# Performance work log

Measured on AMD Instinct MI355X. Metric: run time of the kernel, lower is better.

## Reference

```python
import jax, jax.numpy as jnp
import numpy as np

DIM = 1024
INTER = 512
E = 16            # n_routed_experts
TOPK = 4          # n_activated_experts
N_GROUPS = 4
TOPK_GROUPS = 2
ROUTE_SCALE = 1.0
INIT_STD = 0.02
B, S = 2, 1024


def setup_inputs() -> dict:
    key = jax.random.key(0)
    ks = jax.random.split(key, 8)
    return {
        "x": jax.random.normal(ks[0], (B, S, DIM), jnp.float32),
        "gate_w": jax.random.normal(ks[1], (E, DIM), jnp.float32) * INIT_STD,
        "gate_bias": jnp.zeros((E,), jnp.float32),
        "w1": jax.random.normal(ks[2], (E, INTER, DIM), jnp.float32) * INIT_STD,
        "w2": jax.random.normal(ks[3], (E, DIM, INTER), jnp.float32) * INIT_STD,
        "w3": jax.random.normal(ks[4], (E, INTER, DIM), jnp.float32) * INIT_STD,
        "ws1": jax.random.normal(ks[5], (INTER, DIM), jnp.float32) * INIT_STD,
        "ws2": jax.random.normal(ks[6], (DIM, INTER), jnp.float32) * INIT_STD,
        "ws3": jax.random.normal(ks[7], (INTER, DIM), jnp.float32) * INIT_STD,
    }


def reference(x, gate_w, gate_bias, w1, w2, w3, ws1, ws2, ws3):
    Bx, Sx, D = x.shape
    T = Bx * Sx
    xf = x.reshape(T, D)

    # ---- Gate: sigmoid scores + expert bias, group-limited top-k ----
    scores = jax.nn.sigmoid(xf @ gate_w.T)          # [T, E]
    original_scores = scores
    s = scores + gate_bias                          # bias only affects selection
    sg = s.reshape(T, N_GROUPS, E // N_GROUPS)
    group_scores = sg.max(axis=-1)                  # [T, G]
    _, gidx = jax.lax.top_k(group_scores, TOPK_GROUPS)
    keep = jnp.zeros((T, N_GROUPS), bool).at[jnp.arange(T)[:, None], gidx].set(True)
    s_masked = jnp.where(keep[:, :, None], sg, -jnp.inf).reshape(T, E)
    _, idx = jax.lax.top_k(s_masked, TOPK)          # [T, topk]
    weights = jnp.take_along_axis(original_scores, idx, axis=1) * ROUTE_SCALE

    # combine weights as sparse [T, E] matrix (scatter of top-k weights)
    comb = jnp.zeros((T, E), x.dtype).at[jnp.arange(T)[:, None], idx].add(weights)

    # ---- Routed experts: SwiGLU per expert, weighted combine ----
    h1 = jnp.einsum('td,eid->tei', xf, w1)          # [T, E, inter]
    h3 = jnp.einsum('td,eid->tei', xf, w3)
    h = jax.nn.silu(h1) * h3
    y = jnp.einsum('tei,edi,te->td', h, w2, comb)   # weighted combine

    # ---- Shared expert (SwiGLU MLP) ----
    z = (jax.nn.silu(xf @ ws1.T) * (xf @ ws3.T)) @ ws2.T

    return (y + z).reshape(Bx, Sx, D)
```

## Files before the change

### kernel.cpp

```cpp
#include <hip/hip_runtime.h>

#define T_TOK  2048
#define DIMD   1024
#define INTERI 512
#define NEXP   16
#define NSEG   17

typedef __bf16 bf16x8 __attribute__((ext_vector_type(8)));
typedef float  f32x4  __attribute__((ext_vector_type(4)));

__device__ __forceinline__ unsigned short f2b(float f) {
    union { float f; unsigned int u; } c; c.f = f;
    unsigned int u = c.u;
    unsigned int r = (u + 0x7FFFu + ((u >> 16) & 1u)) >> 16;
    return (unsigned short)r;
}

__device__ __forceinline__ void lds_barrier() {
    asm volatile("s_waitcnt lgkmcnt(0)" ::: "memory");
    __builtin_amdgcn_s_barrier();
}

__global__ __launch_bounds__(256) void cvt_all_kernel(
    const float* __restrict__ x,  const float* __restrict__ w1,
    const float* __restrict__ w3, const float* __restrict__ w2,
    const float* __restrict__ ws1, const float* __restrict__ ws3,
    const float* __restrict__ ws2,
    unsigned short* __restrict__ xb,  unsigned short* __restrict__ w1b,
    unsigned short* __restrict__ w3b, unsigned short* __restrict__ w2b,
    unsigned short* __restrict__ ws1b, unsigned short* __restrict__ ws3b,
    unsigned short* __restrict__ ws2b)
{
    int g = blockIdx.x * 256 + threadIdx.x;
    const float* s; unsigned short* d; int i;
    if      (g < 524288)  { s = x;   d = xb;   i = g; }
    else if (g < 2621440) { s = w1;  d = w1b;  i = g - 524288; }
    else if (g < 4718592) { s = w3;  d = w3b;  i = g - 2621440; }
    else if (g < 6815744) { s = w2;  d = w2b;  i = g - 4718592; }
    else if (g < 6946816) { s = ws1; d = ws1b; i = g - 6815744; }
    else if (g < 7077888) { s = ws3; d = ws3b; i = g - 6946816; }
    else                  { s = ws2; d = ws2b; i = g - 7077888; }
    float4 v = ((const float4*)s)[i];
    ushort4 o;
    o.x = f2b(v.x); o.y = f2b(v.y); o.z = f2b(v.z); o.w = f2b(v.w);
    ((ushort4*)d)[i] = o;
}

__global__ __launch_bounds__(256) void gate_score_kernel(
    const float* __restrict__ x, const float* __restrict__ gw,
    const float* __restrict__ gb,
    unsigned* __restrict__ sel, float4* __restrict__ selw)
{
    int tok  = blockIdx.x * 4 + (threadIdx.x >> 6);
    int lane = threadIdx.x & 63;
    const float* xp = x + (size_t)tok * DIMD;
    float xv[16];
#pragma unroll
    for (int j = 0; j < 16; ++j) xv[j] = xp[j * 64 + lane];

    float sc[16];
#pragma unroll
    for (int e = 0; e < 16; ++e) {
        const float* gwe = gw + e * DIMD;
        float p0 = 0.f, p1 = 0.f;
#pragma unroll
        for (int j = 0; j < 16; j += 2) {
            p0 += xv[j]     * gwe[j * 64 + lane];
            p1 += xv[j + 1] * gwe[(j + 1) * 64 + lane];
        }
        float p = p0 + p1;
#pragma unroll
        for (int o = 32; o; o >>= 1) p += __shfl_xor(p, o, 64);
        sc[e] = p;
    }
    if (lane != 0) return;

    float orig[16], s[16];
#pragma unroll
    for (int e = 0; e < 16; ++e) {
        orig[e] = 1.f / (1.f + expf(-sc[e]));
        s[e] = orig[e] + gb[e];
    }
    float gmax[4];
#pragma unroll
    for (int g = 0; g < 4; ++g) {
        float m = s[4 * g];
        for (int j = 1; j < 4; ++j) m = fmaxf(m, s[4 * g + j]);
        gmax[g] = m;
    }
    int g0 = 0;
    for (int g = 1; g < 4; ++g) if (gmax[g] > gmax[g0]) g0 = g;
    int g1 = -1;
    for (int g = 0; g < 4; ++g) { if (g == g0) continue; if (g1 < 0 || gmax[g] > gmax[g1]) g1 = g; }
    unsigned keep = (0xFu << (4 * g0)) | (0xFu << (4 * g1));
    unsigned used = 0;
    unsigned pk = 0;
    float w4[4];
    for (int j = 0; j < 4; ++j) {
        int best = -1;
        for (int e = 0; e < 16; ++e) {
            if (!((keep >> e) & 1u) || ((used >> e) & 1u)) continue;
            if (best < 0 || s[e] > s[best]) best = e;
        }
        used |= 1u << best;
        pk |= ((unsigned)best) << (4 * j);
        w4[j] = orig[best];
    }
    sel[tok] = pk;
    selw[tok] = make_float4(w4[0], w4[1], w4[2], w4[3]);
}

__global__ __launch_bounds__(256) void build_lists_kernel(
    const unsigned* __restrict__ sel, const float4* __restrict__ selw,
    int* __restrict__ counts, int* __restrict__ lst, float* __restrict__ lstw)
{
    const int e    = blockIdx.x;
    const int tid  = threadIdx.x;
    const int wave = tid >> 6;
    const int lane = tid & 63;

    __shared__ int wsum[4];
    __shared__ int basev;
    if (tid == 0) basev = 0;
    __syncthreads();

    for (int c = 0; c < T_TOK / 256; ++c) {
        int t = c * 256 + tid;
        unsigned s = sel[t];
        int match = -1;
#pragma unroll
        for (int j = 0; j < 4; ++j)
            if (((s >> (4 * j)) & 15u) == (unsigned)e) match = j;
        unsigned long long m = __ballot(match >= 0);
        int wpre = __popcll(m & ((1ull << lane) - 1ull));
        if (lane == 0) wsum[wave] = __popcll(m);
        __syncthreads();
        int pre = basev;
        for (int wv = 0; wv < wave; ++wv) pre += wsum[wv];
        if (match >= 0) {
            int pos = pre + wpre;
            lst [e * T_TOK + pos] = t | (match << 16);
            const float* wp = (const float*)&selw[t];
            lstw[e * T_TOK + pos] = wp[match];
        }
        __syncthreads();
        if (tid == 0) basev += wsum[0] + wsum[1] + wsum[2] + wsum[3];
        __syncthreads();
    }
    if (tid == 0) counts[e] = basev;
}

__global__ __launch_bounds__(256, 4) void gemm1_kernel(
    const unsigned short* __restrict__ xb,
    const unsigned short* __restrict__ w1b,
    const unsigned short* __restrict__ w3b,
    const unsigned short* __restrict__ ws1b,
    const unsigned short* __restrict__ ws3b,
    const int* __restrict__ counts,
    const int* __restrict__ lst,
    unsigned short* __restrict__ H)
{
    int b = blockIdx.x;
    int seg, mt, nt;
    if (b < 2048) {
        int xcd = b & 7, slot = b >> 3;
        seg = xcd + 8 * (slot >> 7);
        int tile = slot & 127;
        nt = tile & 3; mt = tile >> 2;
    } else {
        seg = NEXP;
        int tile = b - 2048;
        nt = tile & 3; mt = tile >> 2;
    }
    const int n_e = (seg == NEXP) ? T_TOK : counts[seg];
    const int m0  = mt * 64;
    if (m0 >= n_e) return;
    const int n0  = nt * 128;

    const unsigned short* w1p = (seg == NEXP) ? ws1b : w1b + (size_t)seg * INTERI * DIMD;
    const unsigned short* w3p = (seg == NEXP) ? ws3b : w3b + (size_t)seg * INTERI * DIMD;
    const int* lste = lst + seg * T_TOK;

    __shared__ __align__(16) unsigned short lA [2][64][32];
    __shared__ __align__(16) unsigned short lB1[2][128][32];
    __shared__ __align__(16) unsigned short lB3[2][128][32];

    const int tid  = threadIdx.x;
    const int wave = tid >> 6;
    const int lane = tid & 63;
    const int r4   = tid >> 2;
    const int skg  = (tid & 3) * 8;

    int ra = m0 + r4; if (ra > n_e - 1) ra = n_e - 1;
    int tok = (seg == NEXP) ? ra : (lste[ra] & 0xFFFF);
    const unsigned short* gA   = xb  + (size_t)tok * DIMD + skg;
    const unsigned short* gB1a = w1p + (size_t)(n0 + r4) * DIMD + skg;
    const unsigned short* gB1b = w1p + (size_t)(n0 + r4 + 64) * DIMD + skg;
    const unsigned short* gB3a = w3p + (size_t)(n0 + r4) * DIMD + skg;
    const unsigned short* gB3b = w3p + (size_t)(n0 + r4 + 64) * DIMD + skg;

    bf16x8 pa[2], pb1a[2], pb1b[2], pb3a[2], pb3b[2];

#define G1LOAD(k0) do { _Pragma("unroll") for (int kk = 0; kk < 2; ++kk) { \
    pa  [kk] = *(const bf16x8*)(gA   + (k0) + kk * 32); \
    pb1a[kk] = *(const bf16x8*)(gB1a + (k0) + kk * 32); \
    pb1b[kk] = *(const bf16x8*)(gB1b + (k0) + kk * 32); \
    pb3a[kk] = *(const bf16x8*)(gB3a + (k0) + kk * 32); \
    pb3b[kk] = *(const bf16x8*)(gB3b + (k0) + kk * 32); } } while (0)

#define G1STORE() do { _Pragma("unroll") for (int kk = 0; kk < 2; ++kk) { \
    *(bf16x8*)&lA [kk][r4][skg]      = pa  [kk]; \
    *(bf16x8*)&lB1[kk][r4][skg]      = pb1a[kk]; \
    *(bf16x8*)&lB1[kk][64 + r4][skg] = pb1b[kk]; \
    *(bf16x8*)&lB3[kk][r4][skg]      = pb3a[kk]; \
    *(bf16x8*)&lB3[kk][64 + r4][skg] = pb3b[kk]; } } while (0)

    f32x4 acc1[2][4], acc3[2][4];
    const f32x4 zero = {0.f, 0.f, 0.f, 0.f};
#pragma unroll
    for (int i = 0; i < 2; ++i)
#pragma unroll
        for (int j = 0; j < 4; ++j) { acc1[i][j] = zero; acc3[i][j] = zero; }

    const int wm   = (wave & 1) * 32;
    const int wn   = (wave >> 1) * 64;
    const int quad = lane >> 4;
    const int lrow = lane & 15;

    G1LOAD(0);
    const int NK = DIMD / 64;
    for (int it = 0; it < NK; ++it) {
        G1STORE();
        lds_barrier();
        if (it + 1 < NK) G1LOAD((it + 1) * 64);
#pragma unroll
        for (int kk = 0; kk < 2; ++kk) {
            bf16x8 a[2], b1[4], b3[4];
#pragma unroll
            for (int t = 0; t < 2; ++t)
                a[t] = *(const bf16x8*)&lA[kk][wm + t * 16 + lrow][quad * 8];
#pragma unroll
            for (int t = 0; t < 4; ++t) {
                b1[t] = *(const bf16x8*)&lB1[kk][wn + t * 16 + lrow][quad * 8];
                b3[t] = *(const bf16x8*)&lB3[kk][wn + t * 16 + lrow][quad * 8];
            }
#pragma unroll
            for (int i = 0; i < 2; ++i)
#pragma unroll
                for (int j = 0; j < 4; ++j) {
                    acc1[i][j] = __builtin_amdgcn_mfma_f32_16x16x32_bf16(a[i], b1[j], acc1[i][j], 0, 0, 0);
                    acc3[i][j] = __builtin_amdgcn_mfma_f32_16x16x32_bf16(a[i], b3[j], acc3[i][j], 0, 0, 0);
                }
        }
        lds_barrier();
    }
#undef G1LOAD
#undef G1STORE

    unsigned short* Hseg = H + (size_t)seg * T_TOK * INTERI;
#pragma unroll
    for (int i = 0; i < 2; ++i) {
        int rbase = m0 + wm + i * 16 + quad * 4;
#pragma unroll
        for (int r = 0; r < 4; ++r) {
            int row = rbase + r;
            if (row >= n_e) continue;
            unsigned short* hrow = Hseg + (size_t)row * INTERI + n0 + wn + lrow;
#pragma unroll
            for (int j = 0; j < 4; ++j) {
                float v1 = acc1[i][j][r];
                float v3 = acc3[i][j][r];
                float hv = (v1 / (1.f + __expf(-v1))) * v3;
                hrow[j * 16] = f2b(hv);
            }
        }
    }
}

__global__ __launch_bounds__(256, 4) void gemm2_kernel(
    const unsigned short* __restrict__ H,
    const unsigned short* __restrict__ w2b,
    const unsigned short* __restrict__ ws2b,
    const int* __restrict__ counts,
    const int* __restrict__ lst,
    const float* __restrict__ lstw,
    float* __restrict__ P)
{
    int b = blockIdx.x;
    int seg, mt, nt;
    if (b < 4096) {
        int xcd = b & 7, slot = b >> 3;
        seg = xcd + 8 * (slot >> 8);
        int tile = slot & 255;
        nt = tile & 7; mt = tile >> 3;
    } else {
        seg = NEXP;
        int tile = b - 4096;
        nt = tile & 7; mt = tile >> 3;
    }
    const int n_e = (seg == NEXP) ? T_TOK : counts[seg];
    const int m0  = mt * 64;
    if (m0 >= n_e) return;
    const int n0  = nt * 128;

    const unsigned short* w2p  = (seg == NEXP) ? ws2b : w2b + (size_t)seg * DIMD * INTERI;
    const unsigned short* Hseg = H + (size_t)seg * T_TOK * INTERI;

    __shared__ __align__(16) unsigned short lA[2][64][32];
    __shared__ __align__(16) unsigned short lB[2][128][32];

    const int tid  = threadIdx.x;
    const int wave = tid >> 6;
    const int lane = tid & 63;
    const int r4   = tid >> 2;
    const int skg  = (tid & 3) * 8;

    int ra = m0 + r4; if (ra > n_e - 1) ra = n_e - 1;
    const unsigned short* gA  = Hseg + (size_t)ra * INTERI + skg;
    const unsigned short* gB0 = w2p + (size_t)(n0 + r4) * INTERI + skg;
    const unsigned short* gB1 = w2p + (size_t)(n0 + r4 + 64) * INTERI + skg;

    bf16x8 pa[2], pb0[2], pb1[2];

#define G2LOAD(k0) do { _Pragma("unroll") for (int kk = 0; kk < 2; ++kk) { \
    pa [kk] = *(const bf16x8*)(gA  + (k0) + kk * 32); \
    pb0[kk] = *(const bf16x8*)(gB0 + (k0) + kk * 32); \
    pb1[kk] = *(const bf16x8*)(gB1 + (k0) + kk * 32); } } while (0)

#define G2STORE() do { _Pragma("unroll") for (int kk = 0; kk < 2; ++kk) { \
    *(bf16x8*)&lA[kk][r4][skg]      = pa [kk]; \
    *(bf16x8*)&lB[kk][r4][skg]      = pb0[kk]; \
    *(bf16x8*)&lB[kk][64 + r4][skg] = pb1[kk]; } } while (0)

    f32x4 acc[2][4];
    const f32x4 zero = {0.f, 0.f, 0.f, 0.f};
#pragma unroll
    for (int i = 0; i < 2; ++i)
#pragma unroll
        for (int j = 0; j < 4; ++j) acc[i][j] = zero;

    const int wm   = (wave & 1) * 32;
    const int wn   = (wave >> 1) * 64;
    const int quad = lane >> 4;
    const int lrow = lane & 15;

    G2LOAD(0);
    const int NK = INTERI / 64;
    for (int it = 0; it < NK; ++it) {
        G2STORE();
        lds_barrier();
        if (it + 1 < NK) G2LOAD((it + 1) * 64);
#pragma unroll
        for (int kk = 0; kk < 2; ++kk) {
            bf16x8 a[2], bv[4];
#pragma unroll
            for (int t = 0; t < 2; ++t)
                a[t] = *(const bf16x8*)&lA[kk][wm + t * 16 + lrow][quad * 8];
#pragma unroll
            for (int t = 0; t < 4; ++t)
                bv[t] = *(const bf16x8*)&lB[kk][wn + t * 16 + lrow][quad * 8];
#pragma unroll
            for (int i = 0; i < 2; ++i)
#pragma unroll
                for (int j = 0; j < 4; ++j)
                    acc[i][j] = __builtin_amdgcn_mfma_f32_16x16x32_bf16(a[i], bv[j], acc[i][j], 0, 0, 0);
        }
        lds_barrier();
    }
#undef G2LOAD
#undef G2STORE

#pragma unroll
    for (int i = 0; i < 2; ++i) {
        int rbase = m0 + wm + i * 16 + quad * 4;
#pragma unroll
        for (int r = 0; r < 4; ++r) {
            int row = rbase + r;
            if (row >= n_e) continue;
            int tok, slot; float wt;
            if (seg == NEXP) { tok = row; slot = 4; wt = 1.f; }
            else {
                int ent = lst[seg * T_TOK + row];
                tok = ent & 0xFFFF; slot = ent >> 16;
                wt = lstw[seg * T_TOK + row];
            }
            float* prow = P + ((size_t)slot * T_TOK + tok) * DIMD + n0 + wn + lrow;
#pragma unroll
            for (int j = 0; j < 4; ++j)
                prow[j * 16] = wt * acc[i][j][r];
        }
    }
}

__global__ __launch_bounds__(256) void combine_kernel(
    const float4* __restrict__ P, float4* __restrict__ y)
{
    const int i = blockIdx.x * 256 + threadIdx.x;
    const size_t plane = (size_t)T_TOK * DIMD / 4;
    float4 a = P[i];
    float4 b = P[plane + i];
    float4 c = P[2 * plane + i];
    float4 d = P[3 * plane + i];
    float4 e = P[4 * plane + i];
    float4 o;
    o.x = a.x + b.x + c.x + d.x + e.x;
    o.y = a.y + b.y + c.y + d.y + e.y;
    o.z = a.z + b.z + c.z + d.z + e.z;
    o.w = a.w + b.w + c.w + d.w + e.w;
    y[i] = o;
}

extern "C" void kernel_launch(void* const* d_in, const int* in_sizes, int n_in,
                              void* d_out, int out_size, void* d_ws, size_t ws_size,
                              hipStream_t stream)
{
    const float* x   = (const float*)d_in[0];
    const float* gw  = (const float*)d_in[1];
    const float* gb  = (const float*)d_in[2];
    const float* w1  = (const float*)d_in[3];
    const float* w2  = (const float*)d_in[4];
    const float* w3  = (const float*)d_in[5];
    const float* ws1 = (const float*)d_in[6];
    const float* ws2 = (const float*)d_in[7];
    const float* ws3 = (const float*)d_in[8];

    char* base = (char*)d_ws;
    size_t off = 0;
    auto alloc = [&](size_t bytes) {
        char* q = base + off; off += (bytes + 255) & ~(size_t)255; return q;
    };
    unsigned short* xb   = (unsigned short*)alloc((size_t)T_TOK * DIMD * 2);
    unsigned short* w1b  = (unsigned short*)alloc((size_t)NEXP * INTERI * DIMD * 2);
    unsigned short* w3b  = (unsigned short*)alloc((size_t)NEXP * INTERI * DIMD * 2);
    unsigned short* w2b  = (unsigned short*)alloc((size_t)NEXP * DIMD * INTERI * 2);
    unsigned short* ws1b = (unsigned short*)alloc((size_t)INTERI * DIMD * 2);
    unsigned short* ws3b = (unsigned short*)alloc((size_t)INTERI * DIMD * 2);
    unsigned short* ws2b = (unsigned short*)alloc((size_t)DIMD * INTERI * 2);
    unsigned short* Hb   = (unsigned short*)alloc((size_t)NSEG * T_TOK * INTERI * 2);
    int*            cnts = (int*)alloc(NEXP * 4);
    int*            lstp = (int*)alloc((size_t)NEXP * T_TOK * 4);
    float*          lstw = (float*)alloc((size_t)NEXP * T_TOK * 4);
    unsigned*       selp = (unsigned*)alloc((size_t)T_TOK * 4);
    float4*         selw = (float4*)alloc((size_t)T_TOK * 16);
    float*          Pb   = (float*)alloc((size_t)5 * T_TOK * DIMD * 4);

    cvt_all_kernel<<<28160, 256, 0, stream>>>(x, w1, w3, w2, ws1, ws3, ws2,
                                              xb, w1b, w3b, w2b, ws1b, ws3b, ws2b);
    gate_score_kernel<<<T_TOK / 4, 256, 0, stream>>>(x, gw, gb, selp, selw);
    build_lists_kernel<<<NEXP, 256, 0, stream>>>(selp, selw, cnts, lstp, lstw);
    gemm1_kernel<<<2176, 256, 0, stream>>>(xb, w1b, w3b, ws1b, ws3b, cnts, lstp, Hb);
    gemm2_kernel<<<4352, 256, 0, stream>>>(Hb, w2b, ws2b, cnts, lstp, lstw, Pb);
    combine_kernel<<<(T_TOK * DIMD / 4) / 256, 256, 0, stream>>>((const float4*)Pb, (float4*)d_out);
}
```

Baseline: 257.8 us.

## Enlarge GEMM M-tile to 128 rows and swizzle LDS columns

Both grouped GEMMs move from 64x128 to 128x128 block tiles, so each wave computes a 64x64 sub-tile with twice the accumulators. The aim is more reuse of each weight tile loaded into LDS and fewer redundant weight reads from global memory. An XOR-style swizzle on the 8-element LDS column groups is added to cut bank conflicts on the fragment reads. The cost is higher register pressure (launch bounds occupancy lowered from 4 to 2), half as many blocks, and more wasted work on partially filled tiles for experts with few tokens.

```diff
diff --git a/kernel.cpp b/kernel.cpp
--- a/kernel.cpp
+++ b/kernel.cpp
@@ -8,6 +8,8 @@
 
 typedef __bf16 bf16x8 __attribute__((ext_vector_type(8)));
 typedef float  f32x4  __attribute__((ext_vector_type(4)));
+
+#define SW(row, c) ((((c) + ((row) >> 1)) & 3) * 8)
 
 __device__ __forceinline__ unsigned short f2b(float f) {
     union { float f; unsigned int u; } c; c.f = f;
@@ -150,7 +152,7 @@
     if (tid == 0) counts[e] = basev;
 }
 
-__global__ __launch_bounds__(256, 4) void gemm1_kernel(
+__global__ __launch_bounds__(256, 2) void gemm1_kernel(
     const unsigned short* __restrict__ xb,
     const unsigned short* __restrict__ w1b,
     const unsigned short* __restrict__ w3b,
@@ -162,18 +164,18 @@
 {
     int b = blockIdx.x;
     int seg, mt, nt;
-    if (b < 2048) {
+    if (b < 1024) {
         int xcd = b & 7, slot = b >> 3;
-        seg = xcd + 8 * (slot >> 7);
-        int tile = slot & 127;
-        nt = tile & 3; mt = tile >> 2;
+        seg = xcd + 8 * (slot >> 6);
+        int tile = slot & 63;
+        mt = tile >> 2; nt = tile & 3;
     } else {
         seg = NEXP;
-        int tile = b - 2048;
-        nt = tile & 3; mt = tile >> 2;
+        int tile = b - 1024;
+        mt = tile >> 2; nt = tile & 3;
     }
     const int n_e = (seg == NEXP) ? T_TOK : counts[seg];
-    const int m0  = mt * 64;
+    const int m0  = mt * 128;
     if (m0 >= n_e) return;
     const int n0  = nt * 128;
 
@@ -181,51 +183,56 @@
     const unsigned short* w3p = (seg == NEXP) ? ws3b : w3b + (size_t)seg * INTERI * DIMD;
     const int* lste = lst + seg * T_TOK;
 
-    __shared__ __align__(16) unsigned short lA [2][64][32];
+    __shared__ __align__(16) unsigned short lA [2][128][32];
     __shared__ __align__(16) unsigned short lB1[2][128][32];
     __shared__ __align__(16) unsigned short lB3[2][128][32];
 
     const int tid  = threadIdx.x;
     const int wave = tid >> 6;
     const int lane = tid & 63;
-    const int r4   = tid >> 2;
-    const int skg  = (tid & 3) * 8;
-
-    int ra = m0 + r4; if (ra > n_e - 1) ra = n_e - 1;
-    int tok = (seg == NEXP) ? ra : (lste[ra] & 0xFFFF);
-    const unsigned short* gA   = xb  + (size_t)tok * DIMD + skg;
-    const unsigned short* gB1a = w1p + (size_t)(n0 + r4) * DIMD + skg;
-    const unsigned short* gB1b = w1p + (size_t)(n0 + r4 + 64) * DIMD + skg;
-    const unsigned short* gB3a = w3p + (size_t)(n0 + r4) * DIMD + skg;
-    const unsigned short* gB3b = w3p + (size_t)(n0 + r4 + 64) * DIMD + skg;
-
-    bf16x8 pa[2], pb1a[2], pb1b[2], pb3a[2], pb3b[2];
-
-#define G1LOAD(k0) do { _Pragma("unroll") for (int kk = 0; kk < 2; ++kk) { \
-    pa  [kk] = *(const bf16x8*)(gA   + (k0) + kk * 32); \
-    pb1a[kk] = *(const bf16x8*)(gB1a + (k0) + kk * 32); \
-    pb1b[kk] = *(const bf16x8*)(gB1b + (k0) + kk * 32); \
-    pb3a[kk] = *(const bf16x8*)(gB3a + (k0) + kk * 32); \
-    pb3b[kk] = *(const bf16x8*)(gB3b + (k0) + kk * 32); } } while (0)
-
-#define G1STORE() do { _Pragma("unroll") for (int kk = 0; kk < 2; ++kk) { \
-    *(bf16x8*)&lA [kk][r4][skg]      = pa  [kk]; \
-    *(bf16x8*)&lB1[kk][r4][skg]      = pb1a[kk]; \
-    *(bf16x8*)&lB1[kk][64 + r4][skg] = pb1b[kk]; \
-    *(bf16x8*)&lB3[kk][r4][skg]      = pb3a[kk]; \
-    *(bf16x8*)&lB3[kk][64 + r4][skg] = pb3b[kk]; } } while (0)
-
-    f32x4 acc1[2][4], acc3[2][4];
-    const f32x4 zero = {0.f, 0.f, 0.f, 0.f};
-#pragma unroll
-    for (int i = 0; i < 2; ++i)
-#pragma unroll
-        for (int j = 0; j < 4; ++j) { acc1[i][j] = zero; acc3[i][j] = zero; }
-
-    const int wm   = (wave & 1) * 32;
-    const int wn   = (wave >> 1) * 64;
     const int quad = lane >> 4;
     const int lrow = lane & 15;
+    const int r4   = tid >> 2;
+    const int ct   = tid & 3;
+
+    int ra0 = m0 + r4;       if (ra0 > n_e - 1) ra0 = n_e - 1;
+    int ra1 = m0 + r4 + 64;  if (ra1 > n_e - 1) ra1 = n_e - 1;
+    int tok0 = (seg == NEXP) ? ra0 : (lste[ra0] & 0xFFFF);
+    int tok1 = (seg == NEXP) ? ra1 : (lste[ra1] & 0xFFFF);
+    const unsigned short* gA0  = xb  + (size_t)tok0 * DIMD + ct * 8;
+    const unsigned short* gA1  = xb  + (size_t)tok1 * DIMD + ct * 8;
+    const unsigned short* gB1a = w1p + (size_t)(n0 + r4)      * DIMD + ct * 8;
+    const unsigned short* gB1b = w1p + (size_t)(n0 + r4 + 64) * DIMD + ct * 8;
+    const unsigned short* gB3a = w3p + (size_t)(n0 + r4)      * DIMD + ct * 8;
+    const unsigned short* gB3b = w3p + (size_t)(n0 + r4 + 64) * DIMD + ct * 8;
+
+    bf16x8 pa[2][2], pb1[2][2], pb3[2][2];
+
+#define G1LOAD(k0) do { _Pragma("unroll") for (int kk = 0; kk < 2; ++kk) { \
+    pa [0][kk] = *(const bf16x8*)(gA0  + (k0) + kk * 32); \
+    pa [1][kk] = *(const bf16x8*)(gA1  + (k0) + kk * 32); \
+    pb1[0][kk] = *(const bf16x8*)(gB1a + (k0) + kk * 32); \
+    pb1[1][kk] = *(const bf16x8*)(gB1b + (k0) + kk * 32); \
+    pb3[0][kk] = *(const bf16x8*)(gB3a + (k0) + kk * 32); \
+    pb3[1][kk] = *(const bf16x8*)(gB3b + (k0) + kk * 32); } } while (0)
+
+#define G1STORE() do { _Pragma("unroll") for (int kk = 0; kk < 2; ++kk) { \
+    *(bf16x8*)&lA [kk][r4]     [SW(r4, ct)]      = pa [0][kk]; \
+    *(bf16x8*)&lA [kk][64 + r4][SW(64 + r4, ct)] = pa [1][kk]; \
+    *(bf16x8*)&lB1[kk][r4]     [SW(r4, ct)]      = pb1[0][kk]; \
+    *(bf16x8*)&lB1[kk][64 + r4][SW(64 + r4, ct)] = pb1[1][kk]; \
+    *(bf16x8*)&lB3[kk][r4]     [SW(r4, ct)]      = pb3[0][kk]; \
+    *(bf16x8*)&lB3[kk][64 + r4][SW(64 + r4, ct)] = pb3[1][kk]; } } while (0)
+
+    f32x4 acc1[4][4], acc3[4][4];
+    const f32x4 zero = {0.f, 0.f, 0.f, 0.f};
+#pragma unroll
+    for (int i = 0; i < 4; ++i)
+#pragma unroll
+        for (int j = 0; j < 4; ++j) { acc1[i][j] = zero; acc3[i][j] = zero; }
+
+    const int wm = (wave & 1) * 64;
+    const int wn = (wave >> 1) * 64;
 
     G1LOAD(0);
     const int NK = DIMD / 64;
@@ -235,17 +242,20 @@
         if (it + 1 < NK) G1LOAD((it + 1) * 64);
 #pragma unroll
         for (int kk = 0; kk < 2; ++kk) {
-            bf16x8 a[2], b1[4], b3[4];
-#pragma unroll
-            for (int t = 0; t < 2; ++t)
-                a[t] = *(const bf16x8*)&lA[kk][wm + t * 16 + lrow][quad * 8];
+            bf16x8 a[4], b1[4], b3[4];
 #pragma unroll
             for (int t = 0; t < 4; ++t) {
-                b1[t] = *(const bf16x8*)&lB1[kk][wn + t * 16 + lrow][quad * 8];
-                b3[t] = *(const bf16x8*)&lB3[kk][wn + t * 16 + lrow][quad * 8];
-            }
-#pragma unroll
-            for (int i = 0; i < 2; ++i)
+                int rr = wm + t * 16 + lrow;
+                a[t] = *(const bf16x8*)&lA[kk][rr][SW(rr, quad)];
+            }
+#pragma unroll
+            for (int t = 0; t < 4; ++t) {
+                int rc = wn + t * 16 + lrow;
+                b1[t] = *(const bf16x8*)&lB1[kk][rc][SW(rc, quad)];
+                b3[t] = *(const bf16x8*)&lB3[kk][rc][SW(rc, quad)];
+            }
+#pragma unroll
+            for (int i = 0; i < 4; ++i)
 #pragma unroll
                 for (int j = 0; j < 4; ++j) {
                     acc1[i][j] = __builtin_amdgcn_mfma_f32_16x16x32_bf16(a[i], b1[j], acc1[i][j], 0, 0, 0);
@@ -259,7 +269,7 @@
 
     unsigned short* Hseg = H + (size_t)seg * T_TOK * INTERI;
 #pragma unroll
-    for (int i = 0; i < 2; ++i) {
+    for (int i = 0; i < 4; ++i) {
         int rbase = m0 + wm + i * 16 + quad * 4;
 #pragma unroll
         for (int r = 0; r < 4; ++r) {
@@ -277,7 +287,7 @@
     }
 }
 
-__global__ __launch_bounds__(256, 4) void gemm2_kernel(
+__global__ __launch_bounds__(256, 2) void gemm2_kernel(
     const unsigned short* __restrict__ H,
     const unsigned short* __restrict__ w2b,
     const unsigned short* __restrict__ ws2b,
@@ -288,61 +298,65 @@
 {
     int b = blockIdx.x;
     int seg, mt, nt;
-    if (b < 4096) {
+    if (b < 2048) {
         int xcd = b & 7, slot = b >> 3;
-        seg = xcd + 8 * (slot >> 8);
-        int tile = slot & 255;
-        nt = tile & 7; mt = tile >> 3;
+        seg = xcd + 8 * (slot >> 7);
+        int tile = slot & 127;
+        mt = tile >> 3; nt = tile & 7;
     } else {
         seg = NEXP;
-        int tile = b - 4096;
-        nt = tile & 7; mt = tile >> 3;
+        int tile = b - 2048;
+        mt = tile >> 3; nt = tile & 7;
     }
     const int n_e = (seg == NEXP) ? T_TOK : counts[seg];
-    const int m0  = mt * 64;
+    const int m0  = mt * 128;
     if (m0 >= n_e) return;
     const int n0  = nt * 128;
 
     const unsigned short* w2p  = (seg == NEXP) ? ws2b : w2b + (size_t)seg * DIMD * INTERI;
     const unsigned short* Hseg = H + (size_t)seg * T_TOK * INTERI;
 
-    __shared__ __align__(16) unsigned short lA[2][64][32];
+    __shared__ __align__(16) unsigned short lA[2][128][32];
     __shared__ __align__(16) unsigned short lB[2][128][32];
 
     const int tid  = threadIdx.x;
     const int wave = tid >> 6;
     const int lane = tid & 63;
-    const int r4   = tid >> 2;
-    const int skg  = (tid & 3) * 8;
-
-    int ra = m0 + r4; if (ra > n_e - 1) ra = n_e - 1;
-    const unsigned short* gA  = Hseg + (size_t)ra * INTERI + skg;
-    const unsigned short* gB0 = w2p + (size_t)(n0 + r4) * INTERI + skg;
-    const unsigned short* gB1 = w2p + (size_t)(n0 + r4 + 64) * INTERI + skg;
-
-    bf16x8 pa[2], pb0[2], pb1[2];
-
-#define G2LOAD(k0) do { _Pragma("unroll") for (int kk = 0; kk < 2; ++kk) { \
-    pa [kk] = *(const bf16x8*)(gA  + (k0) + kk * 32); \
-    pb0[kk] = *(const bf16x8*)(gB0 + (k0) + kk * 32); \
-    pb1[kk] = *(const bf16x8*)(gB1 + (k0) + kk * 32); } } while (0)
-
-#define G2STORE() do { _Pragma("unroll") for (int kk = 0; kk < 2; ++kk) { \
-    *(bf16x8*)&lA[kk][r4][skg]      = pa [kk]; \
-    *(bf16x8*)&lB[kk][r4][skg]      = pb0[kk]; \
-    *(bf16x8*)&lB[kk][64 + r4][skg] = pb1[kk]; } } while (0)
-
-    f32x4 acc[2][4];
-    const f32x4 zero = {0.f, 0.f, 0.f, 0.f};
-#pragma unroll
-    for (int i = 0; i < 2; ++i)
-#pragma unroll
-        for (int j = 0; j < 4; ++j) acc[i][j] = zero;
-
-    const int wm   = (wave & 1) * 32;
-    const int wn   = (wave >> 1) * 64;
     const int quad = lane >> 4;
     const int lrow = lane & 15;
+    const int r4   = tid >> 2;
+    const int ct   = tid & 3;
+
+    int ra0 = m0 + r4;       if (ra0 > n_e - 1) ra0 = n_e - 1;
+    int ra1 = m0 + r4 + 64;  if (ra1 > n_e - 1) ra1 = n_e - 1;
+    const unsigned short* gA0 = Hseg + (size_t)ra0 * INTERI + ct * 8;
+    const unsigned short* gA1 = Hseg + (size_t)ra1 * INTERI + ct * 8;
+    const unsigned short* gB0 = w2p + (size_t)(n0 + r4)      * INTERI + ct * 8;
+    const unsigned short* gB1 = w2p + (size_t)(n0 + r4 + 64) * INTERI + ct * 8;
+
+    bf16x8 pa[2][2], pb[2][2];
+
+#define G2LOAD(k0) do { _Pragma("unroll") for (int kk = 0; kk < 2; ++kk) { \
+    pa[0][kk] = *(const bf16x8*)(gA0 + (k0) + kk * 32); \
+    pa[1][kk] = *(const bf16x8*)(gA1 + (k0) + kk * 32); \
+    pb[0][kk] = *(const bf16x8*)(gB0 + (k0) + kk * 32); \
+    pb[1][kk] = *(const bf16x8*)(gB1 + (k0) + kk * 32); } } while (0)
+
+#define G2STORE() do { _Pragma("unroll") for (int kk = 0; kk < 2; ++kk) { \
+    *(bf16x8*)&lA[kk][r4]     [SW(r4, ct)]      = pa[0][kk]; \
+    *(bf16x8*)&lA[kk][64 + r4][SW(64 + r4, ct)] = pa[1][kk]; \
+    *(bf16x8*)&lB[kk][r4]     [SW(r4, ct)]      = pb[0][kk]; \
+    *(bf16x8*)&lB[kk][64 + r4][SW(64 + r4, ct)] = pb[1][kk]; } } while (0)
+
+    f32x4 acc[4][4];
+    const f32x4 zero = {0.f, 0.f, 0.f, 0.f};
+#pragma unroll
+    for (int i = 0; i < 4; ++i)
+#pragma unroll
+        for (int j = 0; j < 4; ++j) acc[i][j] = zero;
+
+    const int wm = (wave & 1) * 64;
+    const int wn = (wave >> 1) * 64;
 
     G2LOAD(0);
     const int NK = INTERI / 64;
@@ -352,15 +366,19 @@
         if (it + 1 < NK) G2LOAD((it + 1) * 64);
 #pragma unroll
         for (int kk = 0; kk < 2; ++kk) {
-            bf16x8 a[2], bv[4];
-#pragma unroll
-            for (int t = 0; t < 2; ++t)
-                a[t] = *(const bf16x8*)&lA[kk][wm + t * 16 + lrow][quad * 8];
-#pragma unroll
-            for (int t = 0; t < 4; ++t)
-                bv[t] = *(const bf16x8*)&lB[kk][wn + t * 16 + lrow][quad * 8];
-#pragma unroll
-            for (int i = 0; i < 2; ++i)
+            bf16x8 a[4], bv[4];
+#pragma unroll
+            for (int t = 0; t < 4; ++t) {
+                int rr = wm + t * 16 + lrow;
+                a[t] = *(const bf16x8*)&lA[kk][rr][SW(rr, quad)];
+            }
+#pragma unroll
+            for (int t = 0; t < 4; ++t) {
+                int rc = wn + t * 16 + lrow;
+                bv[t] = *(const bf16x8*)&lB[kk][rc][SW(rc, quad)];
+            }
+#pragma unroll
+            for (int i = 0; i < 4; ++i)
 #pragma unroll
                 for (int j = 0; j < 4; ++j)
                     acc[i][j] = __builtin_amdgcn_mfma_f32_16x16x32_bf16(a[i], bv[j], acc[i][j], 0, 0, 0);
@@ -371,7 +389,7 @@
 #undef G2STORE
 
 #pragma unroll
-    for (int i = 0; i < 2; ++i) {
+    for (int i = 0; i < 4; ++i) {
         int rbase = m0 + wm + i * 16 + quad * 4;
 #pragma unroll
         for (int r = 0; r < 4; ++r) {
@@ -448,7 +466,7 @@
                                               xb, w1b, w3b, w2b, ws1b, ws3b, ws2b);
     gate_score_kernel<<<T_TOK / 4, 256, 0, stream>>>(x, gw, gb, selp, selw);
     build_lists_kernel<<<NEXP, 256, 0, stream>>>(selp, selw, cnts, lstp, lstw);
-    gemm1_kernel<<<2176, 256, 0, stream>>>(xb, w1b, w3b, ws1b, ws3b, cnts, lstp, Hb);
-    gemm2_kernel<<<4352, 256, 0, stream>>>(Hb, w2b, ws2b, cnts, lstp, lstw, Pb);
+    gemm1_kernel<<<1088, 256, 0, stream>>>(xb, w1b, w3b, ws1b, ws3b, cnts, lstp, Hb);
+    gemm2_kernel<<<2176, 256, 0, stream>>>(Hb, w2b, ws2b, cnts, lstp, lstw, Pb);
     combine_kernel<<<(T_TOK * DIMD / 4) / 256, 256, 0, stream>>>((const float4*)Pb, (float4*)d_out);
 }
```

Result: faster. 247.7 us (-3.9%).
